# Kernel optimization log

Measured on AMD Instinct MI355X. Metric: run time of the kernel, lower is better.

## Reference

```python
import jax, jax.numpy as jnp
import numpy as np
import math

E = 500_000   # edges
N = 2_000     # nodes (small so duplicate (src,dst) pairs form real groups)
D = 128       # embedding_dim == n_heads*qkv_dim
H = 8         # heads
DK = 16       # qkv_dim
HH = 256      # hyper hidden
EMBD = 2      # hyper embd_dim
CLIP = 10.0   # tanh_clipping


def setup_inputs() -> dict:
    key = jax.random.key(0)
    ks = jax.random.split(key, 12)
    # shared_nodes: inverse indices of unique edge (src,dst) columns (reset() preprocessing)
    rng = np.random.default_rng(0)
    edge_indices = rng.integers(0, N, size=(2, E))
    _, inv = np.unique(edge_indices, axis=1, return_inverse=True)
    shared_nodes = jnp.asarray(inv.reshape(-1), dtype=jnp.int32)

    def lin(k, shape, fan_in):
        return jax.random.normal(k, shape, jnp.float32) / np.sqrt(fan_in)

    return {
        "pref": jax.random.uniform(ks[0], (2,), jnp.float32),
        "dists": jax.random.uniform(ks[1], (E, 2), jnp.float32),
        "edge_emb": jax.random.normal(ks[2], (E, D), jnp.float32),
        "shared_nodes": shared_nodes,
        "fc1_w": lin(ks[3], (HH, 2), 2), "fc1_b": jnp.zeros((HH,), jnp.float32),
        "fc2_w": lin(ks[4], (HH, HH), HH), "fc2_b": jnp.zeros((HH,), jnp.float32),
        "fc3_w": lin(ks[5], (2 * EMBD, HH), HH), "fc3_b": jnp.zeros((2 * EMBD,), jnp.float32),
        "wq_w": lin(ks[6], (D * H * DK, EMBD), EMBD),
        "wk_w": lin(ks[7], (D * H * DK, EMBD), EMBD),
    }


def reference(pref, dists, edge_emb, shared_nodes,
              fc1_w, fc1_b, fc2_w, fc2_b, fc3_w, fc3_b, wq_w, wk_w):
    # --- assign(pref): hypernetwork producing Wq, Wk (no activations, per source) ---
    h = pref @ fc1_w.T + fc1_b
    h = h @ fc2_w.T + fc2_b
    mid = h @ fc3_w.T + fc3_b                    # [4]
    Wq = (mid[:EMBD] @ wq_w.T).reshape(D, H * DK)
    Wk = (mid[EMBD:2 * EMBD] @ wk_w.T).reshape(D, H * DK)

    # --- reset(): scalarized distances + group means over shared edge groups ---
    d = pref[0] * dists[:, 0] + pref[1] * dists[:, 1]   # [E]
    n_edges = edge_emb.shape[0]
    seg = shared_nodes
    group_sums = jax.ops.segment_sum(edge_emb, seg, num_segments=n_edges)
    counts = jax.ops.segment_sum(jnp.ones((n_edges,), edge_emb.dtype), seg,
                                 num_segments=n_edges)
    group_means = group_sums / jnp.clip(counts, 1.0)[:, None]
    q = group_means[seg]                          # [E, D]

    # --- forward(): edge-wise multi-head dot score, tanh clip, group softmax ---
    fq = (q @ Wq.T).reshape(n_edges, H, DK)       # F.linear(q, Wq) (D == H*DK)
    fk = (edge_emb @ Wk.T).reshape(n_edges, H, DK)
    score = (fq * fk).sum(-1).mean(-1) / math.sqrt(D) - d / math.sqrt(2.0)
    score = CLIP * jnp.tanh(score)

    seg_max = jax.ops.segment_max(score, seg, num_segments=n_edges)
    ex = jnp.exp(score - seg_max[seg])
    denom = jax.ops.segment_sum(ex, seg, num_segments=n_edges)
    probs = ex / denom[seg]
    return probs[:, None]                         # [E, 1]
```

## Files before the change

kernel.cpp:

```cpp
#include <hip/hip_runtime.h>
#include <math.h>

#define DD 128
#define HHID 256
#define SLOTS 8


__global__ void k_setup(const float* __restrict__ pref,
                        const float* __restrict__ fc1_w, const float* __restrict__ fc1_b,
                        const float* __restrict__ fc2_w, const float* __restrict__ fc2_b,
                        const float* __restrict__ fc3_w, const float* __restrict__ fc3_b,
                        const float* __restrict__ wq_w, const float* __restrict__ wk_w,
                        const int* __restrict__ seg, unsigned* __restrict__ cs,
                        float* __restrict__ M_, int E_) {
    if (blockIdx.x >= 64) {
        int base = ((int)(blockIdx.x - 64) * blockDim.x + threadIdx.x) * 4;
        if (base + 3 < E_) {
            int4 s4 = *(const int4*)&seg[base];
            atomicAdd(&cs[s4.x], 1u);
            atomicAdd(&cs[s4.y], 1u);
            atomicAdd(&cs[s4.z], 1u);
            atomicAdd(&cs[s4.w], 1u);
        } else {
            for (int e = base; e < E_; ++e) atomicAdd(&cs[seg[e]], 1u);
        }
        return;
    }
    __shared__ float h1[HHID];
    __shared__ float h2[HHID];
    __shared__ float mid[4];
    __shared__ float wqv[2 * DD];
    int t = threadIdx.x;
    float p0 = pref[0], p1 = pref[1];
    h1[t] = fc1_w[t * 2 + 0] * p0 + fc1_w[t * 2 + 1] * p1 + fc1_b[t];
    __syncthreads();
    float acc = fc2_b[t];
    for (int i = 0; i < HHID; ++i) acc += fc2_w[t * HHID + i] * h1[i];
    h2[t] = acc;
    __syncthreads();
    if (t < 4) {
        float m = fc3_b[t];
        for (int i = 0; i < HHID; ++i) m += fc3_w[t * HHID + i] * h2[i];
        mid[t] = m;
    }
    __syncthreads();
    float m0 = mid[0], m1 = mid[1], m2 = mid[2], m3 = mid[3];
    {
        int a = t & 127, rh = t >> 7;
        int r = blockIdx.x * 2 + rh;
        wqv[rh * DD + a] = wq_w[(a * DD + r) * 2 + 0] * m0 + wq_w[(a * DD + r) * 2 + 1] * m1;
    }
    __syncthreads();
    int rh = t >> 7;
    int r = blockIdx.x * 2 + rh;
    int c = t & 127;
    const float scale = 0.011048543456f;
    float s = 0.f;
    for (int a = 0; a < DD; ++a) {
        float wk = wk_w[(a * DD + c) * 2 + 0] * m2 + wk_w[(a * DD + c) * 2 + 1] * m3;
        s += wqv[rh * DD + a] * wk;
    }
    M_[r * DD + c] = s * scale;
}

__global__ void k_classify(const int* __restrict__ seg, unsigned* __restrict__ cs,
                           int* __restrict__ mem, int* __restrict__ glist,
                           int* __restrict__ nctr, float* __restrict__ out, int E_) {
    __shared__ int lcnt;
    __shared__ int lbase;
    int t = threadIdx.x;
    if (t == 0) lcnt = 0;
    __syncthreads();
    int base = (blockIdx.x * blockDim.x + t) * 4;
#define EDGE_STEP(K, G) { unsigned c = cs[(G)] & 0xffffu;                         \
        if (c == 1u) { out[base + (K)] = 1.0f; }                                  \
        else { unsigned old = atomicAdd(&cs[(G)], 0x10000u);                      \
               unsigned j = old >> 16;                                            \
               if (j < SLOTS) mem[(size_t)(G) * SLOTS + j] = base + (K); } }
    if (base + 3 < E_) {
        int4 s4 = *(const int4*)&seg[base];
        EDGE_STEP(0, s4.x) EDGE_STEP(1, s4.y) EDGE_STEP(2, s4.z) EDGE_STEP(3, s4.w)
    } else {
        for (int e = base; e < E_; ++e) {
            int g = seg[e];
            unsigned c = cs[g] & 0xffffu;
            if (c == 1u) { out[e] = 1.0f; }
            else { unsigned old = atomicAdd(&cs[g], 0x10000u);
                   unsigned j = old >> 16;
                   if (j < SLOTS) mem[(size_t)g * SLOTS + j] = e; }
        }
    }
#undef EDGE_STEP
    bool c0 = (base + 0 < E_) && (cs[base + 0] & 0xffffu) >= 2u;
    bool c1 = (base + 1 < E_) && (cs[base + 1] & 0xffffu) >= 2u;
    bool c2 = (base + 2 < E_) && (cs[base + 2] & 0xffffu) >= 2u;
    bool c3 = (base + 3 < E_) && (cs[base + 3] & 0xffffu) >= 2u;
    int m = (int)c0 + (int)c1 + (int)c2 + (int)c3;
    int lpos = 0;
    if (m) lpos = atomicAdd(&lcnt, m);
    __syncthreads();
    if (t == 0 && lcnt) lbase = atomicAdd(&nctr[1], lcnt);
    __syncthreads();
    if (m) {
        int p = lbase + lpos;
        if (c0) glist[p++] = base + 0;
        if (c1) glist[p++] = base + 1;
        if (c2) glist[p++] = base + 2;
        if (c3) glist[p++] = base + 3;
    }
}

__global__ __launch_bounds__(256) void k_fused(const int* __restrict__ glist,
                                               const int* __restrict__ nctr,
                                               const unsigned* __restrict__ cs,
                                               const int* __restrict__ mem,
                                               const float4* __restrict__ M4,
                                               const float4* __restrict__ emb4,
                                               const float2* __restrict__ emb2,
                                               const float2* __restrict__ dists2,
                                               const float* __restrict__ pref,
                                               float* __restrict__ out) {
    __shared__ float meanT[DD * 32];
    __shared__ float gtile[32 * DD];
    int t = threadIdx.x;
    int ng = nctr[1];
    int ntile = (ng + 31) >> 5;
    float p0 = pref[0], p1 = pref[1];
    for (int tile = blockIdx.x; tile < ntile; tile += gridDim.x) {
        int i0 = tile * 32;
        {
            int gi = t & 31;
            int kq = t >> 5;
            int i = i0 + gi;
            float4 s0 = make_float4(0.f, 0.f, 0.f, 0.f), s1 = s0, s2 = s0, s3 = s0;
            float inv = 0.f;
            if (i < ng) {
                int g = glist[i];
                unsigned c = cs[g] & 0xffffu;
                int cm = (int)(c < (unsigned)SLOTS ? c : (unsigned)SLOTS);
                inv = 1.0f / (float)c;
                for (int j = 0; j < cm; ++j) {
                    int e = mem[(size_t)g * SLOTS + j];
                    float4 v0 = emb4[(size_t)e * 32 + kq + 0];
                    float4 v1 = emb4[(size_t)e * 32 + kq + 8];
                    float4 v2 = emb4[(size_t)e * 32 + kq + 16];
                    float4 v3 = emb4[(size_t)e * 32 + kq + 24];
                    s0.x += v0.x; s0.y += v0.y; s0.z += v0.z; s0.w += v0.w;
                    s1.x += v1.x; s1.y += v1.y; s1.z += v1.z; s1.w += v1.w;
                    s2.x += v2.x; s2.y += v2.y; s2.z += v2.z; s2.w += v2.w;
                    s3.x += v3.x; s3.y += v3.y; s3.z += v3.z; s3.w += v3.w;
                }
            }
            int k0 = (kq + 0) * 4, k1 = (kq + 8) * 4, k2 = (kq + 16) * 4, k3 = (kq + 24) * 4;
            meanT[(k0 + 0) * 32 + gi] = s0.x * inv; meanT[(k0 + 1) * 32 + gi] = s0.y * inv;
            meanT[(k0 + 2) * 32 + gi] = s0.z * inv; meanT[(k0 + 3) * 32 + gi] = s0.w * inv;
            meanT[(k1 + 0) * 32 + gi] = s1.x * inv; meanT[(k1 + 1) * 32 + gi] = s1.y * inv;
            meanT[(k1 + 2) * 32 + gi] = s1.z * inv; meanT[(k1 + 3) * 32 + gi] = s1.w * inv;
            meanT[(k2 + 0) * 32 + gi] = s2.x * inv; meanT[(k2 + 1) * 32 + gi] = s2.y * inv;
            meanT[(k2 + 2) * 32 + gi] = s2.z * inv; meanT[(k2 + 3) * 32 + gi] = s2.w * inv;
            meanT[(k3 + 0) * 32 + gi] = s3.x * inv; meanT[(k3 + 1) * 32 + gi] = s3.y * inv;
            meanT[(k3 + 2) * 32 + gi] = s3.z * inv; meanT[(k3 + 3) * 32 + gi] = s3.w * inv;
        }
        __syncthreads();
        {
            int cseg = t & 31;
            int g4 = (t >> 5) * 4;
            float4 acc0 = make_float4(0.f, 0.f, 0.f, 0.f);
            float4 acc1 = acc0, acc2 = acc0, acc3 = acc0;
            #pragma unroll 4
            for (int k = 0; k < DD; ++k) {
                float4 mv = *(const float4*)&meanT[k * 32 + g4];
                float4 Mr = M4[k * 32 + cseg];
                acc0.x += mv.x * Mr.x; acc0.y += mv.x * Mr.y; acc0.z += mv.x * Mr.z; acc0.w += mv.x * Mr.w;
                acc1.x += mv.y * Mr.x; acc1.y += mv.y * Mr.y; acc1.z += mv.y * Mr.z; acc1.w += mv.y * Mr.w;
                acc2.x += mv.z * Mr.x; acc2.y += mv.z * Mr.y; acc2.z += mv.z * Mr.z; acc2.w += mv.z * Mr.w;
                acc3.x += mv.w * Mr.x; acc3.y += mv.w * Mr.y; acc3.z += mv.w * Mr.z; acc3.w += mv.w * Mr.w;
            }
            *(float4*)&gtile[(g4 + 0) * DD + cseg * 4] = acc0;
            *(float4*)&gtile[(g4 + 1) * DD + cseg * 4] = acc1;
            *(float4*)&gtile[(g4 + 2) * DD + cseg * 4] = acc2;
            *(float4*)&gtile[(g4 + 3) * DD + cseg * 4] = acc3;
        }
        __syncthreads();
        {
            int w = t >> 6;
            int lane = t & 63;
            for (int q = 0; q < 8; ++q) {
                int gl = w * 8 + q;
                int i = i0 + gl;
                if (i >= ng) continue;
                int g = glist[i];
                unsigned c = cs[g] & 0xffffu;
                int cm = (int)(c < (unsigned)SLOTS ? c : (unsigned)SLOTS);
                int e_lane = (lane < cm) ? mem[(size_t)g * SLOTS + lane] : 0;
                float2 tv = *(const float2*)&gtile[gl * DD + 2 * lane];
                float s_mine = 0.f;
                for (int j = 0; j < cm; ++j) {
                    int e = __shfl(e_lane, j, 64);
                    float2 kv = emb2[(size_t)e * 64 + lane];
                    float d = tv.x * kv.x + tv.y * kv.y;
                    for (int off = 32; off; off >>= 1) d += __shfl_xor(d, off, 64);
                    if (lane == j) s_mine = d;
                }
                if (lane < cm) {
                    float2 dd = dists2[e_lane];
                    float de = p0 * dd.x + p1 * dd.y;
                    s_mine = 10.0f * tanhf(s_mine - de * 0.7071067811865475f);
                }
                float v = (lane < cm) ? s_mine : -3.0e38f;
                for (int off = 32; off; off >>= 1) v = fmaxf(v, __shfl_xor(v, off, 64));
                float ex = (lane < cm) ? __expf(s_mine - v) : 0.f;
                float sm = ex;
                for (int off = 32; off; off >>= 1) sm += __shfl_xor(sm, off, 64);
                if (lane < cm) out[e_lane] = ex / sm;
            }
        }
        __syncthreads();
    }
}

extern "C" void kernel_launch(void* const* d_in, const int* in_sizes, int n_in,
                              void* d_out, int out_size, void* d_ws, size_t ws_size,
                              hipStream_t stream) {
    const float* pref  = (const float*)d_in[0];
    const float* dists = (const float*)d_in[1];
    const float* emb   = (const float*)d_in[2];
    const int*   seg   = (const int*)d_in[3];
    const float* fc1_w = (const float*)d_in[4];
    const float* fc1_b = (const float*)d_in[5];
    const float* fc2_w = (const float*)d_in[6];
    const float* fc2_b = (const float*)d_in[7];
    const float* fc3_w = (const float*)d_in[8];
    const float* fc3_b = (const float*)d_in[9];
    const float* wq_w  = (const float*)d_in[10];
    const float* wk_w  = (const float*)d_in[11];
    int E_ = in_sizes[3];
    float* out = (float*)d_out;

    char* ws = (char*)d_ws;
    int*      nctr = (int*)ws;
    unsigned* cs   = (unsigned*)(ws + 256);
    size_t zero_bytes = 256 + (size_t)E_ * 4;
    char* p = ws + ((zero_bytes + 255) & ~(size_t)255);
    int*   glist = (int*)p;   p += ((size_t)E_ * 4 + 255) & ~(size_t)255;
    float* M_    = (float*)p; p += (size_t)DD * DD * 4;
    int*   mem   = (int*)p;   p += (size_t)E_ * SLOTS * 4;
    if ((size_t)(p - ws) > ws_size) return;

    hipMemsetAsync(ws, 0, zero_bytes, stream);

    int tb = 256;
    int eb4 = (E_ + tb * 4 - 1) / (tb * 4);
    k_setup<<<64 + eb4, tb, 0, stream>>>(pref, fc1_w, fc1_b, fc2_w, fc2_b, fc3_w, fc3_b,
                                         wq_w, wk_w, seg, cs, M_, E_);
    k_classify<<<eb4, tb, 0, stream>>>(seg, cs, mem, glist, nctr, out, E_);
    k_fused<<<1024, 256, 0, stream>>>(glist, nctr, cs, mem, (const float4*)M_,
                                      (const float4*)emb, (const float2*)emb,
                                      (const float2*)dists, pref, out);
}
```

Measured before the change: 420.9 us.

## Record group member slots during counting pass and pre-fill output with ones

The counting atomics in the setup kernel now return each edge's slot index and write the edge id into the group membership table right away. This removes the second per-edge atomic pass that the classify kernel used to do. The classify kernel becomes a light glist builder that only does vectorised reads of the counts. Singleton outputs are now set by a device memset that fills the whole output with 1.0 before the kernels run. That adds one extra write pass over the output buffer.

```diff
diff --git a/kernel.cpp b/kernel.cpp
--- a/kernel.cpp
+++ b/kernel.cpp
@@ -12,17 +12,25 @@
                         const float* __restrict__ fc3_w, const float* __restrict__ fc3_b,
                         const float* __restrict__ wq_w, const float* __restrict__ wk_w,
                         const int* __restrict__ seg, unsigned* __restrict__ cs,
-                        float* __restrict__ M_, int E_) {
+                        int* __restrict__ mem, float* __restrict__ M_, int E_) {
     if (blockIdx.x >= 64) {
         int base = ((int)(blockIdx.x - 64) * blockDim.x + threadIdx.x) * 4;
         if (base + 3 < E_) {
             int4 s4 = *(const int4*)&seg[base];
-            atomicAdd(&cs[s4.x], 1u);
-            atomicAdd(&cs[s4.y], 1u);
-            atomicAdd(&cs[s4.z], 1u);
-            atomicAdd(&cs[s4.w], 1u);
+            unsigned j0 = atomicAdd(&cs[s4.x], 1u);
+            unsigned j1 = atomicAdd(&cs[s4.y], 1u);
+            unsigned j2 = atomicAdd(&cs[s4.z], 1u);
+            unsigned j3 = atomicAdd(&cs[s4.w], 1u);
+            if (j0 < SLOTS) mem[(size_t)s4.x * SLOTS + j0] = base + 0;
+            if (j1 < SLOTS) mem[(size_t)s4.y * SLOTS + j1] = base + 1;
+            if (j2 < SLOTS) mem[(size_t)s4.z * SLOTS + j2] = base + 2;
+            if (j3 < SLOTS) mem[(size_t)s4.w * SLOTS + j3] = base + 3;
         } else {
-            for (int e = base; e < E_; ++e) atomicAdd(&cs[seg[e]], 1u);
+            for (int e = base; e < E_; ++e) {
+                int g = seg[e];
+                unsigned j = atomicAdd(&cs[g], 1u);
+                if (j < SLOTS) mem[(size_t)g * SLOTS + j] = e;
+            }
         }
         return;
     }
@@ -63,38 +71,24 @@
     M_[r * DD + c] = s * scale;
 }
 
-__global__ void k_classify(const int* __restrict__ seg, unsigned* __restrict__ cs,
-                           int* __restrict__ mem, int* __restrict__ glist,
-                           int* __restrict__ nctr, float* __restrict__ out, int E_) {
+__global__ void k_glist(const unsigned* __restrict__ cs, int* __restrict__ glist,
+                        int* __restrict__ nctr, int E_) {
     __shared__ int lcnt;
     __shared__ int lbase;
     int t = threadIdx.x;
     if (t == 0) lcnt = 0;
     __syncthreads();
     int base = (blockIdx.x * blockDim.x + t) * 4;
-#define EDGE_STEP(K, G) { unsigned c = cs[(G)] & 0xffffu;                         \
-        if (c == 1u) { out[base + (K)] = 1.0f; }                                  \
-        else { unsigned old = atomicAdd(&cs[(G)], 0x10000u);                      \
-               unsigned j = old >> 16;                                            \
-               if (j < SLOTS) mem[(size_t)(G) * SLOTS + j] = base + (K); } }
+    bool c0 = false, c1 = false, c2 = false, c3 = false;
     if (base + 3 < E_) {
-        int4 s4 = *(const int4*)&seg[base];
-        EDGE_STEP(0, s4.x) EDGE_STEP(1, s4.y) EDGE_STEP(2, s4.z) EDGE_STEP(3, s4.w)
+        uint4 c4 = *(const uint4*)&cs[base];
+        c0 = c4.x >= 2u; c1 = c4.y >= 2u; c2 = c4.z >= 2u; c3 = c4.w >= 2u;
     } else {
-        for (int e = base; e < E_; ++e) {
-            int g = seg[e];
-            unsigned c = cs[g] & 0xffffu;
-            if (c == 1u) { out[e] = 1.0f; }
-            else { unsigned old = atomicAdd(&cs[g], 0x10000u);
-                   unsigned j = old >> 16;
-                   if (j < SLOTS) mem[(size_t)g * SLOTS + j] = e; }
-        }
-    }
-#undef EDGE_STEP
-    bool c0 = (base + 0 < E_) && (cs[base + 0] & 0xffffu) >= 2u;
-    bool c1 = (base + 1 < E_) && (cs[base + 1] & 0xffffu) >= 2u;
-    bool c2 = (base + 2 < E_) && (cs[base + 2] & 0xffffu) >= 2u;
-    bool c3 = (base + 3 < E_) && (cs[base + 3] & 0xffffu) >= 2u;
+        if (base + 0 < E_) c0 = cs[base + 0] >= 2u;
+        if (base + 1 < E_) c1 = cs[base + 1] >= 2u;
+        if (base + 2 < E_) c2 = cs[base + 2] >= 2u;
+        if (base + 3 < E_) c3 = cs[base + 3] >= 2u;
+    }
     int m = (int)c0 + (int)c1 + (int)c2 + (int)c3;
     int lpos = 0;
     if (m) lpos = atomicAdd(&lcnt, m);
@@ -136,7 +130,7 @@
             float inv = 0.f;
             if (i < ng) {
                 int g = glist[i];
-                unsigned c = cs[g] & 0xffffu;
+                unsigned c = cs[g];
                 int cm = (int)(c < (unsigned)SLOTS ? c : (unsigned)SLOTS);
                 inv = 1.0f / (float)c;
                 for (int j = 0; j < cm; ++j) {
@@ -190,7 +184,7 @@
                 int i = i0 + gl;
                 if (i >= ng) continue;
                 int g = glist[i];
-                unsigned c = cs[g] & 0xffffu;
+                unsigned c = cs[g];
                 int cm = (int)(c < (unsigned)SLOTS ? c : (unsigned)SLOTS);
                 int e_lane = (lane < cm) ? mem[(size_t)g * SLOTS + lane] : 0;
                 float2 tv = *(const float2*)&gtile[gl * DD + 2 * lane];
@@ -248,12 +242,13 @@
     if ((size_t)(p - ws) > ws_size) return;
 
     hipMemsetAsync(ws, 0, zero_bytes, stream);
+    hipMemsetD32Async((hipDeviceptr_t)out, 0x3f800000u, (size_t)E_, stream);
 
     int tb = 256;
     int eb4 = (E_ + tb * 4 - 1) / (tb * 4);
     k_setup<<<64 + eb4, tb, 0, stream>>>(pref, fc1_w, fc1_b, fc2_w, fc2_b, fc3_w, fc3_b,
-                                         wq_w, wk_w, seg, cs, M_, E_);
-    k_classify<<<eb4, tb, 0, stream>>>(seg, cs, mem, glist, nctr, out, E_);
+                                         wq_w, wk_w, seg, cs, mem, M_, E_);
+    k_glist<<<eb4, tb, 0, stream>>>(cs, glist, nctr, E_);
     k_fused<<<1024, 256, 0, stream>>>(glist, nctr, cs, mem, (const float4*)M_,
                                       (const float4*)emb, (const float2*)emb,
                                       (const float2*)dists, pref, out);
```

Measured after the change: 418.5 us. Within noise of the previous version (-0.6%).
